# Performance work log

Measured on AMD Instinct MI355X. Metric: run time of the kernel, lower is better.

The kernel has to match this reference:

```python
import jax, jax.numpy as jnp
import numpy as np

B, T, NF, D = 32, 128, 20, 512
S = 5            # num_sample
L = 96           # seq_len per utterance (static)
EPS = 1e-8


def _cosine(a, b):
    # torch.F.cosine_similarity: dot / max(|a|*|b|, eps)
    num = jnp.sum(a * b, axis=-1)
    den = jnp.maximum(
        jnp.sqrt(jnp.sum(a * a, axis=-1)) * jnp.sqrt(jnp.sum(b * b, axis=-1)), EPS
    )
    return num / den


def setup_inputs() -> dict:
    key = jax.random.key(0)
    output = jax.random.normal(key, (B, T, NF, D), dtype=jnp.float32)

    # static segment gather indices: seq_len = L for every utterance
    batch_idx = jnp.asarray(np.repeat(np.arange(B), L), dtype=jnp.int32)
    time_idx = jnp.asarray(np.tile(np.arange(L), B), dtype=jnp.int32)

    # negative frame indices: for anchor frame i, sample S frames from
    # {0..NF-1} \ {i-1, i, i+1} (matches masked randperm sampling)
    rng = np.random.default_rng(0)
    neg = np.empty((NF - 1, S), dtype=np.int32)
    all_f = np.arange(NF)
    for i in range(NF - 1):
        allowed = all_f[(all_f != i - 1) & (all_f != i) & (all_f != i + 1)]
        neg[i] = rng.permutation(allowed)[:S]
    neg_idx = jnp.asarray(neg.reshape(-1), dtype=jnp.int32)  # [(NF-1)*S]

    return {"output": output, "batch_idx": batch_idx, "time_idx": time_idx,
            "neg_idx": neg_idx}


def reference(output, batch_idx, time_idx, neg_idx):
    # gather valid segments: [num_seg, NF, D]
    seg = output[batch_idx, time_idx]

    anchors = seg[:, :-1, :]                      # [num_seg, NF-1, D]
    sim_pos = _cosine(anchors, seg[:, 1:, :])     # [num_seg, NF-1]

    # negatives[seg, i, s] = seg[seg, neg_idx[i*S+s]]
    negs = seg[:, neg_idx, :].reshape(seg.shape[0], NF - 1, S, D)
    sim_neg = _cosine(anchors[:, :, None, :], negs)          # [num_seg, NF-1, S]

    sim_all = jnp.concatenate([sim_pos[..., None], sim_neg], axis=-1)
    loss = jnp.mean(-jax.nn.log_softmax(sim_all, axis=-1)[..., 0])
    return loss
```

## Files before the change

### kernel.cpp

```cpp
#include <hip/hip_runtime.h>
#include <hip/hip_bf16.h>
#include <math.h>

#define B_  32
#define T_  128
#define NF_ 20
#define D_  512
#define S_  5
#define L_  96
#define EPS_ 1e-8f
#define NSEG (B_ * L_)
#define NPOS (NF_ - 1)
#define NELEM (NF_ * D_)
#define RPAD (D_ + 8)
#define GLD 33

typedef short short8 __attribute__((ext_vector_type(8)));
typedef float f32x4  __attribute__((ext_vector_type(4)));

__device__ __forceinline__ unsigned short f2bf(float f) {
  unsigned int u = __float_as_uint(f);
  u += 0x7fffu + ((u >> 16) & 1u);
  return (unsigned short)(u >> 16);
}

__global__ __launch_bounds__(256) void phoneme_ssl_seg_kernel(
    const float* __restrict__ out,
    const int* __restrict__ batch_idx,
    const int* __restrict__ time_idx,
    const int* __restrict__ neg_idx,
    float* __restrict__ partials) {

  __shared__ __align__(16) unsigned short V[NF_ * RPAD];
  __shared__ float G[32 * GLD];

  const int n = blockIdx.x;
  const int b = batch_idx[n];
  const int t = time_idx[n];
  const float* __restrict__ src = out + (size_t)(b * T_ + t) * NELEM;

  const float4* __restrict__ src4 = (const float4*)src;
#pragma unroll
  for (int it = 0; it < 5; ++it) {
    const int c = threadIdx.x + 256 * it;
    const float4 x = src4[2 * c];
    const float4 y = src4[2 * c + 1];
    short8 v;
    v[0] = (short)f2bf(x.x); v[1] = (short)f2bf(x.y);
    v[2] = (short)f2bf(x.z); v[3] = (short)f2bf(x.w);
    v[4] = (short)f2bf(y.x); v[5] = (short)f2bf(y.y);
    v[6] = (short)f2bf(y.z); v[7] = (short)f2bf(y.w);
    const int row = c >> 6;
    const int col = (c & 63) * 8;
    *(short8*)&V[row * RPAD + col] = v;
  }
  __syncthreads();
  if (threadIdx.x >= 64) return;

  {
    const int lane = threadIdx.x;
    const int r = lane & 15;
    const int q = lane >> 4;
    const int row1 = (16 + r > 19) ? 19 : 16 + r;
    const unsigned short* p0 = &V[r    * RPAD + q * 8];
    const unsigned short* p1 = &V[row1 * RPAD + q * 8];
    f32x4 c00 = {0.f, 0.f, 0.f, 0.f}, c01 = c00, c10 = c00, c11 = c00;
#pragma unroll
    for (int ks = 0; ks < D_ / 32; ++ks) {
      const short8 a0 = *(const short8*)(p0 + 32 * ks);
      const short8 a1 = *(const short8*)(p1 + 32 * ks);
      c00 = __builtin_amdgcn_mfma_f32_16x16x32_bf16(a0, a0, c00, 0, 0, 0);
      c01 = __builtin_amdgcn_mfma_f32_16x16x32_bf16(a0, a1, c01, 0, 0, 0);
      c10 = __builtin_amdgcn_mfma_f32_16x16x32_bf16(a1, a0, c10, 0, 0, 0);
      c11 = __builtin_amdgcn_mfma_f32_16x16x32_bf16(a1, a1, c11, 0, 0, 0);
    }
#pragma unroll
    for (int reg = 0; reg < 4; ++reg) {
      const int rr = q * 4 + reg;
      G[rr        * GLD + r]      = c00[reg];
      G[rr        * GLD + 16 + r] = c01[reg];
      G[(16 + rr) * GLD + r]      = c10[reg];
      G[(16 + rr) * GLD + 16 + r] = c11[reg];
    }
  }

  float local = 0.f;
  if (threadIdx.x < NPOS) {
    const int i = threadIdx.x;
    const float na = sqrtf(G[i * GLD + i]);
    float sims[1 + S_];
    {
      const float nb = sqrtf(G[(i + 1) * GLD + (i + 1)]);
      sims[0] = G[i * GLD + (i + 1)] / fmaxf(na * nb, EPS_);
    }
#pragma unroll
    for (int j = 0; j < S_; ++j) {
      const int f = neg_idx[i * S_ + j];
      const float nb = sqrtf(G[f * GLD + f]);
      sims[1 + j] = G[i * GLD + f] / fmaxf(na * nb, EPS_);
    }
    float m = sims[0];
#pragma unroll
    for (int j = 1; j < 1 + S_; ++j) m = fmaxf(m, sims[j]);
    float se = 0.f;
#pragma unroll
    for (int j = 0; j < 1 + S_; ++j) se += expf(sims[j] - m);
    const float lse = m + logf(se);
    local = -(sims[0] - lse);
  }

#pragma unroll
  for (int off = 32; off >= 1; off >>= 1)
    local += __shfl_xor(local, off, 64);
  if (threadIdx.x == 0)
    partials[n] = local;
}

__global__ __launch_bounds__(256) void phoneme_ssl_reduce_kernel(
    const float* __restrict__ partials, float* __restrict__ loss_out) {
  float acc = 0.f;
  for (int i = threadIdx.x; i < NSEG; i += 256) acc += partials[i];
#pragma unroll
  for (int off = 32; off >= 1; off >>= 1)
    acc += __shfl_xor(acc, off, 64);
  __shared__ float ws[4];
  if ((threadIdx.x & 63) == 0) ws[threadIdx.x >> 6] = acc;
  __syncthreads();
  if (threadIdx.x == 0)
    loss_out[0] = (ws[0] + ws[1] + ws[2] + ws[3]) * (1.0f / (float)(NSEG * NPOS));
}

extern "C" void kernel_launch(void* const* d_in, const int* in_sizes, int n_in,
                              void* d_out, int out_size, void* d_ws, size_t ws_size,
                              hipStream_t stream) {
  const float* out_t    = (const float*)d_in[0];
  const int* batch_idx  = (const int*)d_in[1];
  const int* time_idx   = (const int*)d_in[2];
  const int* neg_idx    = (const int*)d_in[3];
  float* loss_out       = (float*)d_out;
  float* partials       = (float*)d_ws;

  phoneme_ssl_seg_kernel<<<NSEG, 256, 0, stream>>>(
      out_t, batch_idx, time_idx, neg_idx, partials);
  phoneme_ssl_reduce_kernel<<<1, 256, 0, stream>>>(partials, loss_out);
}
```

Measured before the change: 227.4 us.

## Give each wavefront its own segment and feed MFMA directly from global loads

Instead of one 256-thread block per segment, where all threads stage bf16 rows into LDS and then a single wave runs the MFMA Gram computation, each of the four waves in a block now handles its own segment. Each wave loads fp32 rows straight from global memory into registers, converts them with packed bf16 intrinsics, and feeds the MFMAs with no LDS staging or block-wide barrier. This removes the three idle waves and the shared-memory round trip. The trade-off is that the wave's global loads are now strided per lane and row 19 is reloaded redundantly by the clamped lanes. Negative indices are also prefetched before the matmul.

```diff
diff --git a/kernel.cpp b/kernel.cpp
--- a/kernel.cpp
+++ b/kernel.cpp
@@ -12,16 +12,26 @@
 #define NSEG (B_ * L_)
 #define NPOS (NF_ - 1)
 #define NELEM (NF_ * D_)
-#define RPAD (D_ + 8)
 #define GLD 33
+#define SPB 4
+#define NBLK (NSEG / SPB)
 
 typedef short short8 __attribute__((ext_vector_type(8)));
 typedef float f32x4  __attribute__((ext_vector_type(4)));
 
-__device__ __forceinline__ unsigned short f2bf(float f) {
-  unsigned int u = __float_as_uint(f);
-  u += 0x7fffu + ((u >> 16) & 1u);
-  return (unsigned short)(u >> 16);
+__device__ __forceinline__ unsigned int pkbf16(float lo, float hi) {
+  union { __hip_bfloat162 h; unsigned int u; } r;
+  r.h = __float22bfloat162_rn(make_float2(lo, hi));
+  return r.u;
+}
+
+__device__ __forceinline__ short8 cvt8(const float4 a, const float4 b) {
+  union { short8 v; unsigned int u[4]; } r;
+  r.u[0] = pkbf16(a.x, a.y);
+  r.u[1] = pkbf16(a.z, a.w);
+  r.u[2] = pkbf16(b.x, b.y);
+  r.u[3] = pkbf16(b.z, b.w);
+  return r.v;
 }
 
 __global__ __launch_bounds__(256) void phoneme_ssl_seg_kernel(
@@ -31,73 +41,67 @@
     const int* __restrict__ neg_idx,
     float* __restrict__ partials) {
 
-  __shared__ __align__(16) unsigned short V[NF_ * RPAD];
-  __shared__ float G[32 * GLD];
+  __shared__ float G[SPB * 32 * GLD];
 
-  const int n = blockIdx.x;
+  const int lane = threadIdx.x & 63;
+  const int w    = threadIdx.x >> 6;
+  const int n    = blockIdx.x * SPB + w;
   const int b = batch_idx[n];
   const int t = time_idx[n];
   const float* __restrict__ src = out + (size_t)(b * T_ + t) * NELEM;
 
-  const float4* __restrict__ src4 = (const float4*)src;
+  const int r = lane & 15;
+  const int q = lane >> 4;
+  const int row1 = (16 + r > 19) ? 19 : 16 + r;
+  const float4* __restrict__ p0 = (const float4*)src + (r    * 128 + q * 2);
+  const float4* __restrict__ p1 = (const float4*)src + (row1 * 128 + q * 2);
+
+  int fneg[S_];
+  if (lane < NPOS) {
 #pragma unroll
-  for (int it = 0; it < 5; ++it) {
-    const int c = threadIdx.x + 256 * it;
-    const float4 x = src4[2 * c];
-    const float4 y = src4[2 * c + 1];
-    short8 v;
-    v[0] = (short)f2bf(x.x); v[1] = (short)f2bf(x.y);
-    v[2] = (short)f2bf(x.z); v[3] = (short)f2bf(x.w);
-    v[4] = (short)f2bf(y.x); v[5] = (short)f2bf(y.y);
-    v[6] = (short)f2bf(y.z); v[7] = (short)f2bf(y.w);
-    const int row = c >> 6;
-    const int col = (c & 63) * 8;
-    *(short8*)&V[row * RPAD + col] = v;
-  }
-  __syncthreads();
-  if (threadIdx.x >= 64) return;
-
-  {
-    const int lane = threadIdx.x;
-    const int r = lane & 15;
-    const int q = lane >> 4;
-    const int row1 = (16 + r > 19) ? 19 : 16 + r;
-    const unsigned short* p0 = &V[r    * RPAD + q * 8];
-    const unsigned short* p1 = &V[row1 * RPAD + q * 8];
-    f32x4 c00 = {0.f, 0.f, 0.f, 0.f}, c01 = c00, c10 = c00, c11 = c00;
-#pragma unroll
-    for (int ks = 0; ks < D_ / 32; ++ks) {
-      const short8 a0 = *(const short8*)(p0 + 32 * ks);
-      const short8 a1 = *(const short8*)(p1 + 32 * ks);
-      c00 = __builtin_amdgcn_mfma_f32_16x16x32_bf16(a0, a0, c00, 0, 0, 0);
-      c01 = __builtin_amdgcn_mfma_f32_16x16x32_bf16(a0, a1, c01, 0, 0, 0);
-      c10 = __builtin_amdgcn_mfma_f32_16x16x32_bf16(a1, a0, c10, 0, 0, 0);
-      c11 = __builtin_amdgcn_mfma_f32_16x16x32_bf16(a1, a1, c11, 0, 0, 0);
-    }
-#pragma unroll
-    for (int reg = 0; reg < 4; ++reg) {
-      const int rr = q * 4 + reg;
-      G[rr        * GLD + r]      = c00[reg];
-      G[rr        * GLD + 16 + r] = c01[reg];
-      G[(16 + rr) * GLD + r]      = c10[reg];
-      G[(16 + rr) * GLD + 16 + r] = c11[reg];
-    }
+    for (int j = 0; j < S_; ++j) fneg[j] = neg_idx[lane * S_ + j];
   }
 
+  f32x4 c00 = {0.f, 0.f, 0.f, 0.f}, c01 = c00, c10 = c00, c11 = c00;
+#pragma unroll
+  for (int ks = 0; ks < D_ / 32; ++ks) {
+    const float4 x0 = p0[8 * ks];
+    const float4 x1 = p0[8 * ks + 1];
+    const float4 y0 = p1[8 * ks];
+    const float4 y1 = p1[8 * ks + 1];
+    const short8 a0 = cvt8(x0, x1);
+    const short8 a1 = cvt8(y0, y1);
+    c00 = __builtin_amdgcn_mfma_f32_16x16x32_bf16(a0, a0, c00, 0, 0, 0);
+    c01 = __builtin_amdgcn_mfma_f32_16x16x32_bf16(a0, a1, c01, 0, 0, 0);
+    c10 = __builtin_amdgcn_mfma_f32_16x16x32_bf16(a1, a0, c10, 0, 0, 0);
+    c11 = __builtin_amdgcn_mfma_f32_16x16x32_bf16(a1, a1, c11, 0, 0, 0);
+  }
+
+  float* __restrict__ Gw = G + w * (32 * GLD);
+#pragma unroll
+  for (int reg = 0; reg < 4; ++reg) {
+    const int rr = q * 4 + reg;
+    Gw[rr        * GLD + r]      = c00[reg];
+    Gw[rr        * GLD + 16 + r] = c01[reg];
+    Gw[(16 + rr) * GLD + r]      = c10[reg];
+    Gw[(16 + rr) * GLD + 16 + r] = c11[reg];
+  }
+  __threadfence_block();
+
   float local = 0.f;
-  if (threadIdx.x < NPOS) {
-    const int i = threadIdx.x;
-    const float na = sqrtf(G[i * GLD + i]);
+  if (lane < NPOS) {
+    const int i = lane;
+    const float na = sqrtf(Gw[i * GLD + i]);
     float sims[1 + S_];
     {
-      const float nb = sqrtf(G[(i + 1) * GLD + (i + 1)]);
-      sims[0] = G[i * GLD + (i + 1)] / fmaxf(na * nb, EPS_);
+      const float nb = sqrtf(Gw[(i + 1) * GLD + (i + 1)]);
+      sims[0] = Gw[i * GLD + (i + 1)] / fmaxf(na * nb, EPS_);
     }
 #pragma unroll
     for (int j = 0; j < S_; ++j) {
-      const int f = neg_idx[i * S_ + j];
-      const float nb = sqrtf(G[f * GLD + f]);
-      sims[1 + j] = G[i * GLD + f] / fmaxf(na * nb, EPS_);
+      const int f = fneg[j];
+      const float nb = sqrtf(Gw[f * GLD + f]);
+      sims[1 + j] = Gw[i * GLD + f] / fmaxf(na * nb, EPS_);
     }
     float m = sims[0];
 #pragma unroll
@@ -112,8 +116,7 @@
 #pragma unroll
   for (int off = 32; off >= 1; off >>= 1)
     local += __shfl_xor(local, off, 64);
-  if (threadIdx.x == 0)
-    partials[n] = local;
+  if (lane == 0) partials[n] = local;
 }
 
 __global__ __launch_bounds__(256) void phoneme_ssl_reduce_kernel(
@@ -140,7 +143,7 @@
   float* loss_out       = (float*)d_out;
   float* partials       = (float*)d_ws;
 
-  phoneme_ssl_seg_kernel<<<NSEG, 256, 0, stream>>>(
+  phoneme_ssl_seg_kernel<<<NBLK, 256, 0, stream>>>(
       out_t, batch_idx, time_idx, neg_idx, partials);
   phoneme_ssl_reduce_kernel<<<1, 256, 0, stream>>>(partials, loss_out);
 }
```

New measurement: 230.8 us. About the same (+1.5%).
